# Kernel tuning notes

Hardware: AMD Instinct MI355X
Metric: run time of the kernel (lower is better)

## Reference

```python
import jax, jax.numpy as jnp
import numpy as np

B, S, IN_C, OUT_C = 2, 1024, 4096, 32000


def setup_inputs() -> dict:
    key = jax.random.key(0)
    k1, k2, k3 = jax.random.split(key, 3)
    hidden_states = jax.random.normal(k1, (B, S, IN_C), dtype=jnp.float32)
    weight = jax.random.normal(k2, (OUT_C, IN_C), dtype=jnp.float32) * 0.02
    bias = jax.random.normal(k3, (OUT_C,), dtype=jnp.float32) * 0.02
    return {"hidden_states": hidden_states, "weight": weight, "bias": bias,
            "split_num": 2}


def reference(hidden_states, weight, bias, split_num):
    # SlicedLMHead: split in_features into `split_num` contiguous slices,
    # run each slice as a linear to outC, accumulate, then add bias.
    in_c = hidden_states.shape[-1]
    split_size = in_c // split_num // 2 * 2
    logits = None
    for i in range(split_num):
        start = i * split_size
        end = (i + 1) * split_size if i < split_num - 1 else in_c
        h_slice = hidden_states[:, :, start:end]          # [B, S, slice]
        w_slice = weight[:, start:end]                    # [outC, slice]
        logits_slice = jnp.einsum('bsc,vc->bsv', h_slice, w_slice)
        logits = logits_slice if logits is None else logits + logits_slice
    return logits + bias
```

## Files before the change

kernel.cpp:

```cpp
#include <hip/hip_runtime.h>
#include <hip/hip_bf16.h>


typedef __attribute__((ext_vector_type(8))) short bhalf8;
typedef __attribute__((ext_vector_type(4))) float f32x4;
typedef __attribute__((ext_vector_type(8))) unsigned short us8;

#define M_DIM 2048
#define N_DIM 32000
#define K_DIM 4096
#define BM 128
#define BN 128
#define BK 64
#define NT (K_DIM / BK)
#define MBLKS (M_DIM / BM)
#define NBLKS (N_DIM / BN)
#define NWG   (MBLKS * NBLKS)

#define W_ELEMS ((size_t)N_DIM * K_DIM)
#define H_ELEMS ((size_t)M_DIM * K_DIM)
#define WS_NEEDED ((W_ELEMS + H_ELEMS) * 2)

#define GLOAD_LDS16(g, l) \
    __builtin_amdgcn_global_load_lds( \
        (const __attribute__((address_space(1))) unsigned int*)(g), \
        (__attribute__((address_space(3))) unsigned int*)(l), 16, 0, 0)

__device__ __forceinline__ unsigned short f2bf_rn(float f) {
    unsigned int u = __float_as_uint(f);
    u += 0x7FFFu + ((u >> 16) & 1u);
    return (unsigned short)(u >> 16);
}

__global__ __launch_bounds__(256)
void cvt_f32_bf16(const float* __restrict__ in, unsigned short* __restrict__ out,
                  size_t n8) {
    size_t i = (size_t)blockIdx.x * blockDim.x + threadIdx.x;
    const size_t stride = (size_t)gridDim.x * blockDim.x;
    for (; i < n8; i += stride) {
        const float4 v0 = ((const float4*)in)[i * 2];
        const float4 v1 = ((const float4*)in)[i * 2 + 1];
        us8 p;
        p[0] = f2bf_rn(v0.x); p[1] = f2bf_rn(v0.y);
        p[2] = f2bf_rn(v0.z); p[3] = f2bf_rn(v0.w);
        p[4] = f2bf_rn(v1.x); p[5] = f2bf_rn(v1.y);
        p[6] = f2bf_rn(v1.z); p[7] = f2bf_rn(v1.w);
        ((us8*)out)[i] = p;
    }
}

__global__ __launch_bounds__(256, 3)
void lmhead_gemm_bf16(const unsigned short* __restrict__ A,
                      const unsigned short* __restrict__ W,
                      const float* __restrict__ bias,
                      float* __restrict__ C)
{
    __shared__ unsigned short As[BM * BK];
    __shared__ unsigned short Bs[BN * BK];

    const int tid = threadIdx.x;
    const int bid  = blockIdx.x;
    const int wgid = (bid & 7) * (NWG / 8) + (bid >> 3);
    const int mblk = wgid & (MBLKS - 1);
    const int nblk = wgid >> 4;

    const int lane = tid & 63;
    const int wv   = tid >> 6;
    const int wm   = (wv >> 1) << 6;
    const int wn   = (wv & 1) << 6;
    const int l15  = lane & 15;
    const int l4   = lane >> 4;

    const int st_row = (lane >> 3);
    const int st_g   = lane & 7;

    const unsigned short* srcA[4];
    const unsigned short* srcB[4];
    unsigned short* dstA[4];
    unsigned short* dstB[4];
    #pragma unroll
    for (int i = 0; i < 4; ++i) {
        const int row = (wv * 4 + i) * 8 + st_row;
        const int gsw = (st_g ^ (row & 7)) << 3;
        srcA[i] = A + (size_t)(mblk * BM + row) * K_DIM + gsw;
        srcB[i] = W + (size_t)(nblk * BN + row) * K_DIM + gsw;
        dstA[i] = &As[(wv * 4 + i) * 512];
        dstB[i] = &Bs[(wv * 4 + i) * 512];
    }

    f32x4 acc[4][4] = {};

    for (int t = 0; t < NT; ++t) {
        #pragma unroll
        for (int i = 0; i < 4; ++i) GLOAD_LDS16(srcA[i], dstA[i]);
        #pragma unroll
        for (int i = 0; i < 4; ++i) GLOAD_LDS16(srcB[i], dstB[i]);
        #pragma unroll
        for (int i = 0; i < 4; ++i) { srcA[i] += BK; srcB[i] += BK; }
        __syncthreads();

        #pragma unroll
        for (int kk = 0; kk < 2; ++kk) {
            bhalf8 af[4], bfv[4];
            #pragma unroll
            for (int mf = 0; mf < 4; ++mf) {
                const int row = wm + mf * 16 + l15;
                const int off = row * BK + ((((kk << 2) + l4) ^ (row & 7)) << 3);
                af[mf] = *(const bhalf8*)&As[off];
            }
            #pragma unroll
            for (int nf = 0; nf < 4; ++nf) {
                const int row = wn + nf * 16 + l15;
                const int off = row * BK + ((((kk << 2) + l4) ^ (row & 7)) << 3);
                bfv[nf] = *(const bhalf8*)&Bs[off];
            }
            #pragma unroll
            for (int mf = 0; mf < 4; ++mf)
                #pragma unroll
                for (int nf = 0; nf < 4; ++nf)
                    acc[mf][nf] = __builtin_amdgcn_mfma_f32_16x16x32_bf16(
                        af[mf], bfv[nf], acc[mf][nf], 0, 0, 0);
        }
        __syncthreads();
    }

    const size_t crow0 = (size_t)(mblk * BM + wm + l4 * 4);
    const int    ccol0 = nblk * BN + wn + l15;
    #pragma unroll
    for (int nf = 0; nf < 4; ++nf) {
        const float bv = bias[ccol0 + nf * 16];
        #pragma unroll
        for (int mf = 0; mf < 4; ++mf) {
            const size_t base = (crow0 + (size_t)mf * 16) * N_DIM + ccol0 + nf * 16;
            #pragma unroll
            for (int r = 0; r < 4; ++r)
                C[base + (size_t)r * N_DIM] = acc[mf][nf][r] + bv;
        }
    }
}

__global__ __launch_bounds__(256, 2)
void lmhead_gemm_f32(const float* __restrict__ A, const float* __restrict__ W,
                     const float* __restrict__ bias, float* __restrict__ C) {
    __shared__ unsigned short As[2][BM * BK];
    __shared__ unsigned short Bs[2][BN * BK];

    const int tid  = threadIdx.x;
    const int bid  = blockIdx.x;
    const int mblk = bid & (MBLKS - 1);
    const int nblk = bid >> 4;
    const int st_row = tid >> 3;
    const int st_g   = tid & 7;
    const int lane = tid & 63;
    const int wv   = tid >> 6;
    const int wm   = (wv >> 1) << 6;
    const int wn   = (wv & 1) << 6;
    const int l15  = lane & 15;
    const int l4   = lane >> 4;

    const float* aptr = A + (size_t)(mblk * BM + st_row) * K_DIM + st_g * 8;
    const float* bptr = W + (size_t)(nblk * BN + st_row) * K_DIM + st_g * 8;

    f32x4 acc[4][4] = {};
    float4 ra[4][2], rb[4][2];

    #pragma unroll
    for (int s = 0; s < 4; ++s) {
        const float* ap = aptr + (size_t)(s * 32) * K_DIM;
        const float* bp = bptr + (size_t)(s * 32) * K_DIM;
        ra[s][0] = *(const float4*)(ap);
        ra[s][1] = *(const float4*)(ap + 4);
        rb[s][0] = *(const float4*)(bp);
        rb[s][1] = *(const float4*)(bp + 4);
    }
    #pragma unroll
    for (int s = 0; s < 4; ++s) {
        const int row = s * 32 + st_row;
        const int off = row * BK + ((st_g ^ (row & 7)) << 3);
        us8 pa, pb;
        #pragma unroll
        for (int j = 0; j < 4; ++j) {
            pa[j]     = f2bf_rn(((const float*)&ra[s][0])[j]);
            pa[j + 4] = f2bf_rn(((const float*)&ra[s][1])[j]);
            pb[j]     = f2bf_rn(((const float*)&rb[s][0])[j]);
            pb[j + 4] = f2bf_rn(((const float*)&rb[s][1])[j]);
        }
        *(us8*)&As[0][off] = pa;
        *(us8*)&Bs[0][off] = pb;
    }
    __syncthreads();

    for (int t = 0; t < NT; ++t) {
        const int cur = t & 1;
        const bool more = (t + 1) < NT;
        if (more) {
            const float* ap = aptr + (size_t)(t + 1) * BK;
            const float* bp = bptr + (size_t)(t + 1) * BK;
            #pragma unroll
            for (int s = 0; s < 4; ++s) {
                ra[s][0] = *(const float4*)(ap + (size_t)(s * 32) * K_DIM);
                ra[s][1] = *(const float4*)(ap + (size_t)(s * 32) * K_DIM + 4);
                rb[s][0] = *(const float4*)(bp + (size_t)(s * 32) * K_DIM);
                rb[s][1] = *(const float4*)(bp + (size_t)(s * 32) * K_DIM + 4);
            }
        }
        const unsigned short* as = As[cur];
        const unsigned short* bs = Bs[cur];
        #pragma unroll
        for (int kk = 0; kk < 2; ++kk) {
            bhalf8 af[4], bfv[4];
            #pragma unroll
            for (int mf = 0; mf < 4; ++mf) {
                const int row = wm + mf * 16 + l15;
                const int off = row * BK + ((((kk << 2) + l4) ^ (row & 7)) << 3);
                af[mf] = *(const bhalf8*)&as[off];
            }
            #pragma unroll
            for (int nf = 0; nf < 4; ++nf) {
                const int row = wn + nf * 16 + l15;
                const int off = row * BK + ((((kk << 2) + l4) ^ (row & 7)) << 3);
                bfv[nf] = *(const bhalf8*)&bs[off];
            }
            #pragma unroll
            for (int mf = 0; mf < 4; ++mf)
                #pragma unroll
                for (int nf = 0; nf < 4; ++nf)
                    acc[mf][nf] = __builtin_amdgcn_mfma_f32_16x16x32_bf16(
                        af[mf], bfv[nf], acc[mf][nf], 0, 0, 0);
        }
        if (more) {
            const int nbuf = cur ^ 1;
            #pragma unroll
            for (int s = 0; s < 4; ++s) {
                const int row = s * 32 + st_row;
                const int off = row * BK + ((st_g ^ (row & 7)) << 3);
                us8 pa, pb;
                #pragma unroll
                for (int j = 0; j < 4; ++j) {
                    pa[j]     = f2bf_rn(((const float*)&ra[s][0])[j]);
                    pa[j + 4] = f2bf_rn(((const float*)&ra[s][1])[j]);
                    pb[j]     = f2bf_rn(((const float*)&rb[s][0])[j]);
                    pb[j + 4] = f2bf_rn(((const float*)&rb[s][1])[j]);
                }
                *(us8*)&As[nbuf][off] = pa;
                *(us8*)&Bs[nbuf][off] = pb;
            }
        }
        __syncthreads();
    }

    const size_t crow0 = (size_t)(mblk * BM + wm + l4 * 4);
    const int    ccol0 = nblk * BN + wn + l15;
    #pragma unroll
    for (int nf = 0; nf < 4; ++nf) {
        const float bv = bias[ccol0 + nf * 16];
        #pragma unroll
        for (int mf = 0; mf < 4; ++mf) {
            const size_t base = (crow0 + (size_t)mf * 16) * N_DIM + ccol0 + nf * 16;
            #pragma unroll
            for (int r = 0; r < 4; ++r)
                C[base + (size_t)r * N_DIM] = acc[mf][nf][r] + bv;
        }
    }
}

extern "C" void kernel_launch(void* const* d_in, const int* in_sizes, int n_in,
                              void* d_out, int out_size, void* d_ws, size_t ws_size,
                              hipStream_t stream) {
    const float* h = (const float*)d_in[0];
    const float* w = (const float*)d_in[1];
    const float* b = (const float*)d_in[2];
    float* out = (float*)d_out;

    if (ws_size >= WS_NEEDED) {
        unsigned short* wbf = (unsigned short*)d_ws;
        unsigned short* hbf = wbf + W_ELEMS;
        cvt_f32_bf16<<<2048, 256, 0, stream>>>(w, wbf, W_ELEMS / 8);
        cvt_f32_bf16<<<512, 256, 0, stream>>>(h, hbf, H_ELEMS / 8);
        lmhead_gemm_bf16<<<NWG, 256, 0, stream>>>(hbf, wbf, b, out);
    } else {
        lmhead_gemm_f32<<<NWG, 256, 0, stream>>>(h, w, b, out);
    }
}
```

Before: 763.8 us.

## Use 256x256 tiles with 8 waves and a software-pipelined double-buffered LDS loop

Replaces the 128x128 bf16 GEMM kernel with a 256x256-tile kernel that runs 512 threads (8 waves) per workgroup and uses a 128KB double-buffered LDS region. Global-to-LDS loads for the next K-steps are issued between four MFMA phases, with explicit waitcnt, barriers and s_setprio so loads overlap compute. The larger tile raises data reuse per loaded byte. The cost is fewer workgroups (1000), a possible tail imbalance across CUs, and one resident workgroup per CU because of the LDS footprint. The f32 fallback path only gets hardcoded constants.

```diff
diff --git a/kernel.cpp b/kernel.cpp
--- a/kernel.cpp
+++ b/kernel.cpp
@@ -9,13 +9,13 @@
 #define M_DIM 2048
 #define N_DIM 32000
 #define K_DIM 4096
-#define BM 128
-#define BN 128
+#define BM 256
+#define BN 256
 #define BK 64
 #define NT (K_DIM / BK)
 #define MBLKS (M_DIM / BM)
 #define NBLKS (N_DIM / BN)
-#define NWG   (MBLKS * NBLKS)
+#define NWG (MBLKS * NBLKS)
 
 #define W_ELEMS ((size_t)N_DIM * K_DIM)
 #define H_ELEMS ((size_t)M_DIM * K_DIM)
@@ -49,105 +49,179 @@
     }
 }
 
-__global__ __launch_bounds__(256, 3)
-void lmhead_gemm_bf16(const unsigned short* __restrict__ A,
-                      const unsigned short* __restrict__ W,
-                      const float* __restrict__ bias,
-                      float* __restrict__ C)
+__global__ __launch_bounds__(512, 2)
+void lmhead_gemm_256(const unsigned short* __restrict__ A,
+                     const unsigned short* __restrict__ W,
+                     const float* __restrict__ bias,
+                     float* __restrict__ C)
 {
-    __shared__ unsigned short As[BM * BK];
-    __shared__ unsigned short Bs[BN * BK];
-
-    const int tid = threadIdx.x;
+    __shared__ unsigned short lds[65536];
+
+    const int tid  = threadIdx.x;
     const int bid  = blockIdx.x;
     const int wgid = (bid & 7) * (NWG / 8) + (bid >> 3);
     const int mblk = wgid & (MBLKS - 1);
-    const int nblk = wgid >> 4;
+    const int nblk = wgid >> 3;
 
     const int lane = tid & 63;
     const int wv   = tid >> 6;
-    const int wm   = (wv >> 1) << 6;
-    const int wn   = (wv & 1) << 6;
+    const int wr   = wv >> 2;
+    const int wc   = wv & 3;
     const int l15  = lane & 15;
     const int l4   = lane >> 4;
 
-    const int st_row = (lane >> 3);
-    const int st_g   = lane & 7;
-
-    const unsigned short* srcA[4];
-    const unsigned short* srcB[4];
-    unsigned short* dstA[4];
-    unsigned short* dstB[4];
+    const int strow = tid >> 3;
+    const int sgsw  = ((tid & 7) ^ (strow & 7)) << 3;
+    const unsigned short* const srcA = A + (size_t)(mblk * BM + strow) * K_DIM + sgsw;
+    const unsigned short* const srcB = W + (size_t)(nblk * BN + strow) * K_DIM + sgsw;
+    const int dstw = (tid & 448) * 8;
+
+#define STAGE_A(u, h) { \
+        const unsigned short* s_ = srcA + (size_t)((h) * 128) * K_DIM + (size_t)(u) * BK; \
+        unsigned short* d_ = &lds[((((u) & 1) * 2 + (h)) * 8192) + dstw]; \
+        GLOAD_LDS16(s_, d_); GLOAD_LDS16(s_ + (size_t)64 * K_DIM, d_ + 4096); }
+#define STAGE_B(u, h) { \
+        const unsigned short* s_ = srcB + (size_t)((h) * 128) * K_DIM + (size_t)(u) * BK; \
+        unsigned short* d_ = &lds[32768 + ((((u) & 1) * 2 + (h)) * 8192) + dstw]; \
+        GLOAD_LDS16(s_, d_); GLOAD_LDS16(s_ + (size_t)64 * K_DIM, d_ + 4096); }
+
+    const int swz0  = (l4 ^ (l15 & 7)) << 3;
+    const int swz1  = ((4 + l4) ^ (l15 & 7)) << 3;
+    const int aoff0 = l15 * 64 + swz0;
+    const int aoff1 = l15 * 64 + swz1;
+    const int boff0 = ((wc & 1) * 64 + l15) * 64 + swz0;
+    const int boff1 = ((wc & 1) * 64 + l15) * 64 + swz1;
+
+    f32x4 acc[8][4] = {};
+    bhalf8 af0[4][2], af1[4][2], bf[4][2];
+
+    STAGE_A(0, 0); STAGE_A(0, 1);
+    STAGE_B(0, 0); STAGE_B(0, 1);
+    STAGE_A(1, 0); STAGE_A(1, 1);
+    asm volatile("s_waitcnt vmcnt(4)" ::: "memory");
+    __builtin_amdgcn_sched_barrier(0);
+    __builtin_amdgcn_s_barrier();
+
+    for (int t = 0; t < NT; ++t) {
+        const int b = t & 1;
+        const unsigned short* asb = &lds[(b * 2 + wr) * 8192];
+        const unsigned short* bsb = &lds[32768 + (b * 2 + (wc >> 1)) * 8192];
+
+        #pragma unroll
+        for (int mf = 0; mf < 4; ++mf) {
+            af0[mf][0] = *(const bhalf8*)&asb[aoff0 + mf * 1024];
+            af0[mf][1] = *(const bhalf8*)&asb[aoff1 + mf * 1024];
+        }
+        #pragma unroll
+        for (int nf = 0; nf < 2; ++nf) {
+            bf[nf][0] = *(const bhalf8*)&bsb[boff0 + nf * 1024];
+            bf[nf][1] = *(const bhalf8*)&bsb[boff1 + nf * 1024];
+        }
+        if (t + 1 < NT) STAGE_B(t + 1, 0);
+        __builtin_amdgcn_sched_barrier(0);
+        __builtin_amdgcn_s_barrier();
+        asm volatile("s_waitcnt lgkmcnt(0)" ::: "memory");
+        __builtin_amdgcn_sched_barrier(0);
+        __builtin_amdgcn_s_setprio(1);
+        #pragma unroll
+        for (int mf = 0; mf < 4; ++mf)
+            #pragma unroll
+            for (int nf = 0; nf < 2; ++nf)
+                #pragma unroll
+                for (int kk = 0; kk < 2; ++kk)
+                    acc[mf][nf] = __builtin_amdgcn_mfma_f32_16x16x32_bf16(
+                        af0[mf][kk], bf[nf][kk], acc[mf][nf], 0, 0, 0);
+        __builtin_amdgcn_s_setprio(0);
+        __builtin_amdgcn_s_barrier();
+
+        #pragma unroll
+        for (int nf = 0; nf < 2; ++nf) {
+            bf[2 + nf][0] = *(const bhalf8*)&bsb[boff0 + (2 + nf) * 1024];
+            bf[2 + nf][1] = *(const bhalf8*)&bsb[boff1 + (2 + nf) * 1024];
+        }
+        if (t + 1 < NT) STAGE_B(t + 1, 1);
+        __builtin_amdgcn_sched_barrier(0);
+        __builtin_amdgcn_s_barrier();
+        asm volatile("s_waitcnt lgkmcnt(0)" ::: "memory");
+        __builtin_amdgcn_sched_barrier(0);
+        __builtin_amdgcn_s_setprio(1);
+        #pragma unroll
+        for (int mf = 0; mf < 4; ++mf)
+            #pragma unroll
+            for (int nf = 0; nf < 2; ++nf)
+                #pragma unroll
+                for (int kk = 0; kk < 2; ++kk)
+                    acc[mf][2 + nf] = __builtin_amdgcn_mfma_f32_16x16x32_bf16(
+                        af0[mf][kk], bf[2 + nf][kk], acc[mf][2 + nf], 0, 0, 0);
+        __builtin_amdgcn_s_setprio(0);
+        __builtin_amdgcn_s_barrier();
+
+        #pragma unroll
+        for (int mf = 0; mf < 4; ++mf) {
+            af1[mf][0] = *(const bhalf8*)&asb[aoff0 + 4096 + mf * 1024];
+            af1[mf][1] = *(const bhalf8*)&asb[aoff1 + 4096 + mf * 1024];
+        }
+        __builtin_amdgcn_sched_barrier(0);
+        __builtin_amdgcn_s_barrier();
+        asm volatile("s_waitcnt lgkmcnt(0)" ::: "memory");
+        __builtin_amdgcn_sched_barrier(0);
+        __builtin_amdgcn_s_setprio(1);
+        #pragma unroll
+        for (int mf = 0; mf < 4; ++mf)
+            #pragma unroll
+            for (int nf = 0; nf < 2; ++nf)
+                #pragma unroll
+                for (int kk = 0; kk < 2; ++kk)
+                    acc[4 + mf][2 + nf] = __builtin_amdgcn_mfma_f32_16x16x32_bf16(
+                        af1[mf][kk], bf[2 + nf][kk], acc[4 + mf][2 + nf], 0, 0, 0);
+        __builtin_amdgcn_s_setprio(0);
+        __builtin_amdgcn_s_barrier();
+
+        if (t + 2 < NT) { STAGE_A(t + 2, 0); STAGE_A(t + 2, 1); }
+        __builtin_amdgcn_sched_barrier(0);
+        __builtin_amdgcn_s_barrier();
+        __builtin_amdgcn_s_setprio(1);
+        #pragma unroll
+        for (int mf = 0; mf < 4; ++mf)
+            #pragma unroll
+            for (int nf = 0; nf < 2; ++nf)
+                #pragma unroll
+                for (int kk = 0; kk < 2; ++kk)
+                    acc[4 + mf][nf] = __builtin_amdgcn_mfma_f32_16x16x32_bf16(
+                        af1[mf][kk], bf[nf][kk], acc[4 + mf][nf], 0, 0, 0);
+        __builtin_amdgcn_s_setprio(0);
+        if (t < NT - 2) { asm volatile("s_waitcnt vmcnt(4)" ::: "memory"); }
+        else            { asm volatile("s_waitcnt vmcnt(0)" ::: "memory"); }
+        __builtin_amdgcn_sched_barrier(0);
+        __builtin_amdgcn_s_barrier();
+    }
+
+    const size_t crow0 = (size_t)(mblk * BM + wr * 128 + l4 * 4);
+    const int    ccol0 = nblk * BN + wc * 64 + l15;
     #pragma unroll
-    for (int i = 0; i < 4; ++i) {
-        const int row = (wv * 4 + i) * 8 + st_row;
-        const int gsw = (st_g ^ (row & 7)) << 3;
-        srcA[i] = A + (size_t)(mblk * BM + row) * K_DIM + gsw;
-        srcB[i] = W + (size_t)(nblk * BN + row) * K_DIM + gsw;
-        dstA[i] = &As[(wv * 4 + i) * 512];
-        dstB[i] = &Bs[(wv * 4 + i) * 512];
-    }
-
-    f32x4 acc[4][4] = {};
-
-    for (int t = 0; t < NT; ++t) {
-        #pragma unroll
-        for (int i = 0; i < 4; ++i) GLOAD_LDS16(srcA[i], dstA[i]);
-        #pragma unroll
-        for (int i = 0; i < 4; ++i) GLOAD_LDS16(srcB[i], dstB[i]);
-        #pragma unroll
-        for (int i = 0; i < 4; ++i) { srcA[i] += BK; srcB[i] += BK; }
-        __syncthreads();
-
-        #pragma unroll
-        for (int kk = 0; kk < 2; ++kk) {
-            bhalf8 af[4], bfv[4];
-            #pragma unroll
-            for (int mf = 0; mf < 4; ++mf) {
-                const int row = wm + mf * 16 + l15;
-                const int off = row * BK + ((((kk << 2) + l4) ^ (row & 7)) << 3);
-                af[mf] = *(const bhalf8*)&As[off];
-            }
-            #pragma unroll
-            for (int nf = 0; nf < 4; ++nf) {
-                const int row = wn + nf * 16 + l15;
-                const int off = row * BK + ((((kk << 2) + l4) ^ (row & 7)) << 3);
-                bfv[nf] = *(const bhalf8*)&Bs[off];
-            }
-            #pragma unroll
-            for (int mf = 0; mf < 4; ++mf)
-                #pragma unroll
-                for (int nf = 0; nf < 4; ++nf)
-                    acc[mf][nf] = __builtin_amdgcn_mfma_f32_16x16x32_bf16(
-                        af[mf], bfv[nf], acc[mf][nf], 0, 0, 0);
-        }
-        __syncthreads();
-    }
-
-    const size_t crow0 = (size_t)(mblk * BM + wm + l4 * 4);
-    const int    ccol0 = nblk * BN + wn + l15;
-    #pragma unroll
-    for (int nf = 0; nf < 4; ++nf) {
-        const float bv = bias[ccol0 + nf * 16];
-        #pragma unroll
-        for (int mf = 0; mf < 4; ++mf) {
-            const size_t base = (crow0 + (size_t)mf * 16) * N_DIM + ccol0 + nf * 16;
+    for (int jn = 0; jn < 4; ++jn) {
+        const float bv = bias[ccol0 + jn * 16];
+        #pragma unroll
+        for (int i = 0; i < 8; ++i) {
+            const size_t base = (crow0 + (size_t)i * 16) * N_DIM + ccol0 + jn * 16;
             #pragma unroll
             for (int r = 0; r < 4; ++r)
-                C[base + (size_t)r * N_DIM] = acc[mf][nf][r] + bv;
-        }
-    }
+                C[base + (size_t)r * N_DIM] = acc[i][jn][r] + bv;
+        }
+    }
+#undef STAGE_A
+#undef STAGE_B
 }
 
 __global__ __launch_bounds__(256, 2)
 void lmhead_gemm_f32(const float* __restrict__ A, const float* __restrict__ W,
                      const float* __restrict__ bias, float* __restrict__ C) {
-    __shared__ unsigned short As[2][BM * BK];
-    __shared__ unsigned short Bs[2][BN * BK];
+    __shared__ unsigned short As[2][128 * 64];
+    __shared__ unsigned short Bs[2][128 * 64];
 
     const int tid  = threadIdx.x;
     const int bid  = blockIdx.x;
-    const int mblk = bid & (MBLKS - 1);
+    const int mblk = bid & 15;
     const int nblk = bid >> 4;
     const int st_row = tid >> 3;
     const int st_g   = tid & 7;
@@ -158,8 +232,8 @@
     const int l15  = lane & 15;
     const int l4   = lane >> 4;
 
-    const float* aptr = A + (size_t)(mblk * BM + st_row) * K_DIM + st_g * 8;
-    const float* bptr = W + (size_t)(nblk * BN + st_row) * K_DIM + st_g * 8;
+    const float* aptr = A + (size_t)(mblk * 128 + st_row) * K_DIM + st_g * 8;
+    const float* bptr = W + (size_t)(nblk * 128 + st_row) * K_DIM + st_g * 8;
 
     f32x4 acc[4][4] = {};
     float4 ra[4][2], rb[4][2];
@@ -168,34 +242,31 @@
     for (int s = 0; s < 4; ++s) {
         const float* ap = aptr + (size_t)(s * 32) * K_DIM;
         const float* bp = bptr + (size_t)(s * 32) * K_DIM;
-        ra[s][0] = *(const float4*)(ap);
-        ra[s][1] = *(const float4*)(ap + 4);
-        rb[s][0] = *(const float4*)(bp);
-        rb[s][1] = *(const float4*)(bp + 4);
+        ra[s][0] = *(const float4*)(ap);   ra[s][1] = *(const float4*)(ap + 4);
+        rb[s][0] = *(const float4*)(bp);   rb[s][1] = *(const float4*)(bp + 4);
     }
     #pragma unroll
     for (int s = 0; s < 4; ++s) {
         const int row = s * 32 + st_row;
-        const int off = row * BK + ((st_g ^ (row & 7)) << 3);
+        const int off = row * 64 + ((st_g ^ (row & 7)) << 3);
         us8 pa, pb;
         #pragma unroll
         for (int j = 0; j < 4; ++j) {
-            pa[j]     = f2bf_rn(((const float*)&ra[s][0])[j]);
+            pa[j] = f2bf_rn(((const float*)&ra[s][0])[j]);
             pa[j + 4] = f2bf_rn(((const float*)&ra[s][1])[j]);
-            pb[j]     = f2bf_rn(((const float*)&rb[s][0])[j]);
+            pb[j] = f2bf_rn(((const float*)&rb[s][0])[j]);
             pb[j + 4] = f2bf_rn(((const float*)&rb[s][1])[j]);
         }
-        *(us8*)&As[0][off] = pa;
-        *(us8*)&Bs[0][off] = pb;
+        *(us8*)&As[0][off] = pa;  *(us8*)&Bs[0][off] = pb;
     }
     __syncthreads();
 
-    for (int t = 0; t < NT; ++t) {
+    for (int t = 0; t < 64; ++t) {
         const int cur = t & 1;
-        const bool more = (t + 1) < NT;
+        const bool more = (t + 1) < 64;
         if (more) {
-            const float* ap = aptr + (size_t)(t + 1) * BK;
-            const float* bp = bptr + (size_t)(t + 1) * BK;
+            const float* ap = aptr + (size_t)(t + 1) * 64;
+            const float* bp = bptr + (size_t)(t + 1) * 64;
             #pragma unroll
             for (int s = 0; s < 4; ++s) {
                 ra[s][0] = *(const float4*)(ap + (size_t)(s * 32) * K_DIM);
@@ -212,14 +283,12 @@
             #pragma unroll
             for (int mf = 0; mf < 4; ++mf) {
                 const int row = wm + mf * 16 + l15;
-                const int off = row * BK + ((((kk << 2) + l4) ^ (row & 7)) << 3);
-                af[mf] = *(const bhalf8*)&as[off];
+                af[mf] = *(const bhalf8*)&as[row * 64 + ((((kk << 2) + l4) ^ (row & 7)) << 3)];
             }
             #pragma unroll
             for (int nf = 0; nf < 4; ++nf) {
                 const int row = wn + nf * 16 + l15;
-                const int off = row * BK + ((((kk << 2) + l4) ^ (row & 7)) << 3);
-                bfv[nf] = *(const bhalf8*)&bs[off];
+                bfv[nf] = *(const bhalf8*)&bs[row * 64 + ((((kk << 2) + l4) ^ (row & 7)) << 3)];
             }
             #pragma unroll
             for (int mf = 0; mf < 4; ++mf)
@@ -233,24 +302,23 @@
             #pragma unroll
             for (int s = 0; s < 4; ++s) {
                 const int row = s * 32 + st_row;
-                const int off = row * BK + ((st_g ^ (row & 7)) << 3);
+                const int off = row * 64 + ((st_g ^ (row & 7)) << 3);
                 us8 pa, pb;
                 #pragma unroll
                 for (int j = 0; j < 4; ++j) {
-                    pa[j]     = f2bf_rn(((const float*)&ra[s][0])[j]);
+                    pa[j] = f2bf_rn(((const float*)&ra[s][0])[j]);
                     pa[j + 4] = f2bf_rn(((const float*)&ra[s][1])[j]);
-                    pb[j]     = f2bf_rn(((const float*)&rb[s][0])[j]);
+                    pb[j] = f2bf_rn(((const float*)&rb[s][0])[j]);
                     pb[j + 4] = f2bf_rn(((const float*)&rb[s][1])[j]);
                 }
-                *(us8*)&As[nbuf][off] = pa;
-                *(us8*)&Bs[nbuf][off] = pb;
+                *(us8*)&As[nbuf][off] = pa;  *(us8*)&Bs[nbuf][off] = pb;
             }
         }
         __syncthreads();
     }
 
-    const size_t crow0 = (size_t)(mblk * BM + wm + l4 * 4);
-    const int    ccol0 = nblk * BN + wn + l15;
+    const size_t crow0 = (size_t)(mblk * 128 + wm + l4 * 4);
+    const int    ccol0 = nblk * 128 + wn + l15;
     #pragma unroll
     for (int nf = 0; nf < 4; ++nf) {
         const float bv = bias[ccol0 + nf * 16];
@@ -277,8 +345,8 @@
         unsigned short* hbf = wbf + W_ELEMS;
         cvt_f32_bf16<<<2048, 256, 0, stream>>>(w, wbf, W_ELEMS / 8);
         cvt_f32_bf16<<<512, 256, 0, stream>>>(h, hbf, H_ELEMS / 8);
-        lmhead_gemm_bf16<<<NWG, 256, 0, stream>>>(hbf, wbf, b, out);
+        lmhead_gemm_256<<<NWG, 512, 0, stream>>>(hbf, wbf, b, out);
     } else {
-        lmhead_gemm_f32<<<NWG, 256, 0, stream>>>(h, w, b, out);
-    }
-}
+        lmhead_gemm_f32<<<4000, 256, 0, stream>>>(h, w, b, out);
+    }
+}
```

New measurement: 629.5 us. -17.6%, faster.
